# Optimization experiments

Hardware: AMD Instinct MI355X
Metric: run time of the kernel (lower is better)

Reference implementation:

```python
import jax, jax.numpy as jnp
import numpy as np

N, C_A, C_S, C_Z, H = 1024, 768, 384, 128, 16
D = C_A // H  # 48


def _ln(x, gamma=None, beta=None, eps=1e-5):
    m = jnp.mean(x, axis=-1, keepdims=True)
    v = jnp.var(x, axis=-1, keepdims=True)
    y = (x - m) * jax.lax.rsqrt(v + eps)
    if gamma is not None:
        y = y * gamma
    if beta is not None:
        y = y + beta
    return y


def _adaln(a, s, gamma_s, Wg, bg, Wadd):
    # AF3 Algorithm 26: LN(a) w/o affine, LN(s) w/ scale only; gate + additive shift from s
    a_ln = _ln(a)
    s_ln = _ln(s, gamma_s)
    return jax.nn.sigmoid(s_ln @ Wg + bg) * a_ln + s_ln @ Wadd


def setup_inputs() -> dict:
    key = jax.random.key(0)
    ks = iter(jax.random.split(key, 40))
    def nrm(shape, scale=0.02):
        return jax.random.normal(next(ks), shape, dtype=jnp.float32) * scale
    f32 = jnp.float32
    return dict(
        a=jax.random.normal(next(ks), (1, N, C_A), dtype=f32),
        s=jax.random.normal(next(ks), (1, N, C_S), dtype=f32),
        z=jax.random.normal(next(ks), (1, N, N, C_Z), dtype=f32),
        # AdaptiveLayerNorm (attention branch)
        gamma_s1=jnp.ones((C_S,), f32), Wg1=nrm((C_S, C_A)), bg1=jnp.zeros((C_A,), f32), Wadd1=nrm((C_S, C_A)),
        # pair-bias: LN(z) scale-only + LinearNoBias(c_z -> n_heads)
        gamma_z=jnp.ones((C_Z,), f32), Wz=nrm((C_Z, H)),
        # Attention: q has bias, k/v no bias, sigmoid gating, output proj
        Wq=nrm((C_A, C_A)), bq=jnp.zeros((C_A,), f32),
        Wk=nrm((C_A, C_A)), Wv=nrm((C_A, C_A)),
        Wgate=nrm((C_A, C_A)), bgate=jnp.ones((C_A,), f32),
        Wo=nrm((C_A, C_A)), bo=jnp.zeros((C_A,), f32),
        # BiasInitLinear output gate (biasinit=-2)
        Ws_last=nrm((C_S, C_A)), bs_last=jnp.full((C_A,), -2.0, f32),
        # ConditionedTransitionBlock (n=2)
        gamma_s2=jnp.ones((C_S,), f32), Wg2=nrm((C_S, C_A)), bg2=jnp.zeros((C_A,), f32), Wadd2=nrm((C_S, C_A)),
        W1=nrm((C_A, 2 * C_A)), W2=nrm((C_A, 2 * C_A)), Wb=nrm((2 * C_A, C_A)),
        Ws_t=nrm((C_S, C_A)), b_t=jnp.full((C_A,), -2.0, f32),
    )


def reference(a, s, z, gamma_s1, Wg1, bg1, Wadd1, gamma_z, Wz,
              Wq, bq, Wk, Wv, Wgate, bgate, Wo, bo, Ws_last, bs_last,
              gamma_s2, Wg2, bg2, Wadd2, W1, W2, Wb, Ws_t, b_t):
    B = a.shape[0]
    # ---- AttentionPairBias (standard / global path) ----
    a_ln = _adaln(a, s, gamma_s1, Wg1, bg1, Wadd1)
    bias = _ln(z, gamma_z) @ Wz                     # [B, N, N, H]
    bias = jnp.moveaxis(bias, -1, -3)               # [B, H, N, N]
    q = (a_ln @ Wq + bq).reshape(B, N, H, D)
    k = (a_ln @ Wk).reshape(B, N, H, D)
    v = (a_ln @ Wv).reshape(B, N, H, D)
    scale = 1.0 / float(np.sqrt(D))
    scores = jnp.einsum('bqhd,bkhd->bhqk', q, k) * scale + bias
    attn = jax.nn.softmax(scores, axis=-1)
    o = jnp.einsum('bhqk,bkhd->bqhd', attn, v)      # [B, N, H, D]
    g = jax.nn.sigmoid(a_ln @ Wgate + bgate).reshape(B, N, H, D)
    o = (g * o).reshape(B, N, C_A) @ Wo + bo
    attn_out = jax.nn.sigmoid(s @ Ws_last + bs_last) * o
    # ---- ConditionedTransitionBlock (Algorithm 25, n=2) ----
    a2 = _adaln(a, s, gamma_s2, Wg2, bg2, Wadd2)
    bmid = jax.nn.silu(a2 @ W1) * (a2 @ W2)
    t_out = jax.nn.sigmoid(s @ Ws_t + b_t) * (bmid @ Wb)
    # Algorithm 23 line 2-3: a = b + ConditionedTransitionBlock(a, s)
    return attn_out + t_out
```

## Files before the change

kernel.cpp:

```cpp
#include <hip/hip_runtime.h>

typedef __bf16 bf16;
typedef __bf16 v8bf __attribute__((ext_vector_type(8)));
typedef float  v4f  __attribute__((ext_vector_type(4)));
typedef short  short4v __attribute__((ext_vector_type(4)));

__device__ __forceinline__ float sigf(float x){ return 1.0f/(1.0f + __expf(-x)); }

typedef __attribute__((address_space(3))) unsigned int lds_u32;
typedef __attribute__((address_space(1))) const unsigned int gbl_u32;
__device__ __forceinline__ void gl16(const void* g, void* l) {
  __builtin_amdgcn_global_load_lds((gbl_u32*)g, (lds_u32*)l, 16, 0, 0);
}

struct WTab {
  const float* src[14];
  bf16* dst[14];
  int K[14], N[14], boff[14];
};

__device__ __forceinline__ void prepw_body(int bid, char* smem, const WTab& tab) {
  float (*lds)[33] = (float(*)[33])smem;
  int e = 0;
  #pragma unroll
  for (int i = 1; i < 14; i++) if (tab.boff[i] <= bid) e = i;
  int local = bid - tab.boff[e];
  int K = tab.K[e], N = tab.N[e];
  int nKT = K >> 5;
  int kt = local % nKT, nt = local / nKT;
  int k0 = kt * 32, n0 = nt * 32;
  const float* src = tab.src[e];
  bf16* dst = tab.dst[e];
  int tx = threadIdx.x & 31, ty = threadIdx.x >> 5;
  #pragma unroll
  for (int i = 0; i < 4; i++)
    lds[ty + i*8][tx] = src[(long)(k0 + ty + i*8) * N + n0 + tx];
  __syncthreads();
  #pragma unroll
  for (int i = 0; i < 4; i++)
    dst[(long)(n0 + ty + i*8) * K + k0 + tx] = (bf16)lds[tx][ty + i*8];
}

__device__ __forceinline__ void ln_a_body(int row, const float* __restrict__ a,
                                          float* __restrict__ out) {
  const float* x = a + (long)row * 768;
  int t = threadIdx.x;
  float lv[3], s = 0.f, q = 0.f;
  #pragma unroll
  for (int i = 0; i < 3; i++){ lv[i] = x[t + i*256]; s += lv[i]; q += lv[i]*lv[i]; }
  #pragma unroll
  for (int m = 1; m < 64; m <<= 1){ s += __shfl_xor(s, m); q += __shfl_xor(q, m); }
  __shared__ float ls[4], lq[4];
  int w = t >> 6, lane = t & 63;
  if (!lane){ ls[w] = s; lq[w] = q; }
  __syncthreads();
  s = ls[0]+ls[1]+ls[2]+ls[3]; q = lq[0]+lq[1]+lq[2]+lq[3];
  float mean = s * (1.f/768.f);
  float var  = q * (1.f/768.f) - mean*mean;
  float inv  = rsqrtf(var + 1e-5f);
  float* o = out + (long)row * 768;
  #pragma unroll
  for (int i = 0; i < 3; i++) o[t + i*256] = (lv[i] - mean) * inv;
}

__device__ __forceinline__ void ln_s_body(int rowpair, const float* __restrict__ sIn,
    const float* __restrict__ g1, const float* __restrict__ g2,
    bf16* __restrict__ s1, bf16* __restrict__ s2, bf16* __restrict__ sb) {
  int t = threadIdx.x & 127;
  int sub = threadIdx.x >> 7;
  int r = rowpair*2 + sub;
  const float* x = sIn + (long)r * 384;
  float lv[3], s = 0.f, q = 0.f;
  #pragma unroll
  for (int i = 0; i < 3; i++){ lv[i] = x[t + i*128]; s += lv[i]; q += lv[i]*lv[i]; }
  #pragma unroll
  for (int m = 1; m < 64; m <<= 1){ s += __shfl_xor(s, m); q += __shfl_xor(q, m); }
  __shared__ float ls[2][2], lq[2][2];
  int w = (t >> 6) & 1, lane = t & 63;
  if (!lane){ ls[sub][w] = s; lq[sub][w] = q; }
  __syncthreads();
  s = ls[sub][0] + ls[sub][1]; q = lq[sub][0] + lq[sub][1];
  float mean = s * (1.f/384.f);
  float var  = q * (1.f/384.f) - mean*mean;
  float inv  = rsqrtf(var + 1e-5f);
  long base = (long)r * 384;
  #pragma unroll
  for (int i = 0; i < 3; i++){
    int c = t + i*128;
    float y = (lv[i] - mean) * inv;
    s1[base + c] = (bf16)(y * g1[c]);
    s2[base + c] = (bf16)(y * g2[c]);
    sb[base + c] = (bf16)lv[i];
  }
}

__global__ __launch_bounds__(256) void k_prep(WTab tab, int boffTot,
    const float* Wz, const float* gz, bf16* wzT,
    const float* A_in, float* alnr,
    const float* S_in, const float* g1, const float* g2,
    bf16* sl1, bf16* sl2, bf16* sbf)
{
  __shared__ __align__(16) char smem[4224];
  int bid = blockIdx.x;
  if (bid < boffTot) { prepw_body(bid, smem, tab); return; }
  bid -= boffTot;
  if (bid < 8) {
    int t = bid * 256 + threadIdx.x;
    int k = t >> 4, h = t & 15;
    wzT[h * 128 + k] = (bf16)(Wz[t] * gz[k]);
    return;
  }
  bid -= 8;
  if (bid < 1024) { ln_a_body(bid, A_in, alnr); return; }
  bid -= 1024;
  ln_s_body(bid, S_in, g1, g2, sl1, sl2, sbf);
}

__device__ __forceinline__ void zbias_body(int bid, char* smem,
    const float* __restrict__ z, const bf16* __restrict__ wzT,
    bf16* __restrict__ biasb) {
  float (*pb)[17] = (float(*)[17])smem;
  int t = threadIdx.x, lane = t & 63, w = t >> 6;
  int r16 = lane & 15, g4 = lane >> 4;
  long base = (long)bid * 64;
  long pos = base + w*16 + r16;
  const float* zr = z + pos * 128;
  float4 xv[8];
  #pragma unroll
  for (int s = 0; s < 4; s++) {
    xv[2*s]   = *reinterpret_cast<const float4*>(&zr[s*32 + g4*8]);
    xv[2*s+1] = *reinterpret_cast<const float4*>(&zr[s*32 + g4*8 + 4]);
  }
  const float* x = reinterpret_cast<const float*>(xv);
  float sm = 0.f, q = 0.f;
  #pragma unroll
  for (int i = 0; i < 32; i++){ sm += x[i]; q += x[i]*x[i]; }
  sm += __shfl_xor(sm, 16); q += __shfl_xor(q, 16);
  sm += __shfl_xor(sm, 32); q += __shfl_xor(q, 32);
  float mean = sm * (1.f/128.f), var = q * (1.f/128.f) - mean*mean;
  float inv = rsqrtf(var + 1e-5f);
  v4f acc = (v4f){0.f, 0.f, 0.f, 0.f};
  #pragma unroll
  for (int s = 0; s < 4; s++) {
    union { bf16 b[8]; v8bf v; } ua;
    #pragma unroll
    for (int j = 0; j < 8; j++) ua.b[j] = (bf16)((x[s*8 + j] - mean) * inv);
    v8bf bw = *reinterpret_cast<const v8bf*>(&wzT[r16*128 + s*32 + g4*8]);
    acc = __builtin_amdgcn_mfma_f32_16x16x32_bf16(ua.v, bw, acc, 0, 0, 0);
  }
  #pragma unroll
  for (int r = 0; r < 4; r++) pb[w*16 + g4*4 + r][r16] = acc[r];
  __syncthreads();
  int p = t & 63, hb = t >> 6;
  #pragma unroll
  for (int j = 0; j < 4; j++) {
    int h = hb*4 + j;
    biasb[((long)h << 20) + base + p] = (bf16)pb[p][h];
  }
}

#define EPI_ADASG  0
#define EPI_SWIGLU 1
#define EPI_QKVG   2
#define EPI_WO     6
#define EPI_WB     7

template<int TM, int TN, bool DUAL, int EPI>
__device__ __forceinline__ void gemm_body(
    bf16* As, bf16* Bs, int m0, int n0, int z,
    const bf16* __restrict__ Ap, const bf16* __restrict__ B1, long sBpair, int K,
    const float* __restrict__ f0, const float* __restrict__ f1,
    const float* __restrict__ f2, const float* __restrict__ f3,
    const float* __restrict__ f4, const bf16* __restrict__ bb0,
    void* __restrict__ outp, long sOutz)
{
  constexpr int WM = TM/2, WN = TN/2;
  constexpr int MI = WM/16, NI = WN/16;
  const bf16* B2 = B1 + sBpair;
  int t = threadIdx.x, lane = t & 63, w = t >> 6;
  int wr = w >> 1, wc = w & 1;
  int r16 = lane & 15, g4 = lane >> 4;
  constexpr int NACC = DUAL ? 2 : 1;
  v4f acc[NACC][MI][NI];
  #pragma unroll
  for (int d = 0; d < NACC; d++)
    #pragma unroll
    for (int mi = 0; mi < MI; mi++)
      #pragma unroll
      for (int ni = 0; ni < NI; ni++)
        acc[d][mi][ni] = (v4f){0.f, 0.f, 0.f, 0.f};

  for (int k0 = 0; k0 < K; k0 += 64) {
    #pragma unroll
    for (int cb = 0; cb < TM/32; cb++) {
      int cc = cb*4 + w;
      int c16 = cc*64 + lane;
      int row = c16 >> 3, col = c16 & 7;
      int scol = col ^ (row & 7);
      gl16(&Ap[(long)(m0 + row)*K + k0 + scol*8], (char*)As + cc*1024);
    }
    #pragma unroll
    for (int cb = 0; cb < TN/32; cb++) {
      int cc = cb*4 + w;
      int c16 = cc*64 + lane;
      int row = c16 >> 3, col = c16 & 7;
      int scol = col ^ (row & 7);
      gl16(&B1[(long)(n0 + row)*K + k0 + scol*8], (char*)Bs + cc*1024);
      if constexpr (DUAL)
        gl16(&B2[(long)(n0 + row)*K + k0 + scol*8], (char*)Bs + TN*128 + cc*1024);
    }
    __syncthreads();
    #pragma unroll
    for (int s = 0; s < 2; s++) {
      int ch = s*4 + g4;
      v8bf af[MI];
      #pragma unroll
      for (int mi = 0; mi < MI; mi++) {
        int ra = wr*WM + mi*16 + r16;
        af[mi] = *reinterpret_cast<const v8bf*>(
            (const char*)As + ra*128 + ((ch ^ (ra & 7)) << 4));
      }
      #pragma unroll
      for (int d = 0; d < NACC; d++)
        #pragma unroll
        for (int ni = 0; ni < NI; ni++) {
          int rb = wc*WN + ni*16 + r16;
          v8bf bfv = *reinterpret_cast<const v8bf*>(
              (const char*)Bs + d*(TN*128) + rb*128 + ((ch ^ (rb & 7)) << 4));
          #pragma unroll
          for (int mi = 0; mi < MI; mi++)
            acc[d][mi][ni] = __builtin_amdgcn_mfma_f32_16x16x32_bf16(af[mi], bfv, acc[d][mi][ni], 0, 0, 0);
        }
    }
    __syncthreads();
  }

  int colb = n0 + wc*WN + r16;
  int rowb = m0 + wr*WM + (g4 << 2);
  #pragma unroll
  for (int mi = 0; mi < MI; mi++)
    #pragma unroll
    for (int ni = 0; ni < NI; ni++) {
      int col = colb + ni*16;
      if constexpr (EPI == EPI_ADASG) {
        if (z < 2) {
          float bg = (z == 0 ? f1 : f2)[col];
          bf16* o = (bf16*)outp + (long)z * sOutz;
          #pragma unroll
          for (int r = 0; r < 4; r++) {
            long idx = (long)(rowb + mi*16 + r)*768 + col;
            float gl = acc[0][mi][ni][r] + bg;
            o[idx] = (bf16)(sigf(gl) * f0[idx] + acc[1][mi][ni][r]);
          }
        } else {
          bf16* o0 = (bf16*)outp + 2*sOutz;
          bf16* o1 = (bf16*)outp + 3*sOutz;
          #pragma unroll
          for (int r = 0; r < 4; r++) {
            long idx = (long)(rowb + mi*16 + r)*768 + col;
            o0[idx] = (bf16)sigf(acc[0][mi][ni][r] + f3[col]);
            o1[idx] = (bf16)sigf(acc[1][mi][ni][r] + f4[col]);
          }
        }
      } else if constexpr (EPI == EPI_SWIGLU) {
        bf16* o = (bf16*)outp;
        #pragma unroll
        for (int r = 0; r < 4; r++) {
          long idx = (long)(rowb + mi*16 + r)*1536 + col;
          float x1 = acc[0][mi][ni][r], x2 = acc[1][mi][ni][r];
          o[idx] = (bf16)(x1 * sigf(x1) * x2);
        }
      } else if constexpr (EPI == EPI_QKVG) {
        int h = col / 48, d = col - h*48;
        if (z == 0) {
          const float qs = 0.14433756729740643f;
          bf16* qp = (bf16*)outp;
          #pragma unroll
          for (int r = 0; r < 4; r++)
            qp[(long)h*65536 + (long)(rowb + mi*16 + r)*64 + d] =
              (bf16)((acc[0][mi][ni][r] + f0[col]) * qs);
        } else if (z == 1) {
          bf16* kp = (bf16*)outp + sOutz;
          #pragma unroll
          for (int r = 0; r < 4; r++)
            kp[(long)h*65536 + (long)(rowb + mi*16 + r)*64 + d] = (bf16)acc[0][mi][ni][r];
        } else if (z == 2) {
          bf16* vT = (bf16*)outp + 2*sOutz;
          union { bf16 h4[4]; short4v s4; } u;
          #pragma unroll
          for (int r = 0; r < 4; r++) u.h4[r] = (bf16)acc[0][mi][ni][r];
          *reinterpret_cast<short4v*>(&vT[(long)h*65536 + (long)d*1024 + rowb + mi*16]) = u.s4;
        } else {
          bf16* gp = (bf16*)outp + 3*sOutz;
          #pragma unroll
          for (int r = 0; r < 4; r++)
            gp[(long)(rowb + mi*16 + r)*768 + col] = (bf16)sigf(acc[0][mi][ni][r] + f1[col]);
        }
      } else if constexpr (EPI == EPI_WO) {
        float* o = (float*)outp;
        #pragma unroll
        for (int r = 0; r < 4; r++) {
          long idx = (long)(rowb + mi*16 + r)*768 + col;
          o[idx] = (float)bb0[idx] * (acc[0][mi][ni][r] + f0[col]);
        }
      } else {
        float* o = (float*)outp;
        #pragma unroll
        for (int r = 0; r < 4; r++) {
          long idx = (long)(rowb + mi*16 + r)*768 + col;
          o[idx] = f0[idx] + (float)bb0[idx] * acc[0][mi][ni][r];
        }
      }
    }
}

template<int TM, int TN, bool DUAL, int EPI>
__global__ __launch_bounds__(256) void gemm_k(
    const bf16* A, const bf16* B, long sAz, long sBz, long sBpair, int K,
    const float* f0, const float* f1, const float* f2, const float* f3,
    const float* f4, const bf16* bb0, void* outp, long sOutz)
{
  __shared__ __align__(16) bf16 As[TM*64];
  __shared__ __align__(16) bf16 Bs[(DUAL?2:1)*TN*64];
  int z = blockIdx.z;
  gemm_body<TM,TN,DUAL,EPI>(As, Bs, blockIdx.y*TM, blockIdx.x*TN, z,
      A + (long)z*sAz, B + (long)z*sBz, sBpair, K,
      f0, f1, f2, f3, f4, bb0, outp, sOutz);
}

#define ZSPLIT 5120

__global__ __launch_bounds__(256, 4) void k_mega_a(
    const bf16* sl1, const bf16* wGA6, const float* alnr,
    const float* bg1, const float* bg2, const float* bsL, const float* b_t,
    bf16* aln, const float* Zin, const bf16* wzT, bf16* biasb)
{
  __shared__ __align__(16) char smem[24576];
  int bid = blockIdx.x;
  if (bid < 576) {
    int z = bid / 192, rem = bid % 192;
    gemm_body<64,64,true,EPI_ADASG>((bf16*)smem, (bf16*)(smem + 8192),
        (rem/12)*64, (rem%12)*64, z,
        sl1 + (long)z*393216, wGA6 + (long)z*589824, 294912, 384,
        alnr, bg1, bg2, bsL, b_t, nullptr, aln, 786432);
  } else {
    zbias_body(bid - 576, smem, Zin, wzT, biasb);
  }
}

__global__ __launch_bounds__(256, 3) void k_mega_b(
    const bf16* aln, const bf16* wQKVG, const float* bq, const float* bgate,
    bf16* qkv, const bf16* a2b, const bf16* wW12, bf16* bmid,
    const float* Zin, const bf16* wzT, bf16* biasb)
{
  __shared__ __align__(16) char smem[32768];
  int bid = blockIdx.x;
  if (bid < 192) {
    int z = bid / 48, rem = bid % 48;
    gemm_body<128,128,false,EPI_QKVG>((bf16*)smem, (bf16*)(smem + 16384),
        (rem/6)*128, (rem%6)*128, z,
        aln, wQKVG + (long)z*589824, 0, 768,
        bq, bgate, nullptr, nullptr, nullptr, nullptr, qkv, 1048576);
  } else if (bid < 576) {
    int rem = bid - 192;
    gemm_body<64,64,true,EPI_SWIGLU>((bf16*)smem, (bf16*)(smem + 8192),
        (rem/24)*64, (rem%24)*64, 0,
        a2b, wW12, 1179648, 768,
        nullptr, nullptr, nullptr, nullptr, nullptr, nullptr, bmid, 0);
  } else {
    zbias_body(bid - 576 + ZSPLIT, smem, Zin, wzT, biasb);
  }
}

__global__ __launch_bounds__(256) void k_flash(
    const bf16* __restrict__ qp, const bf16* __restrict__ kp,
    const bf16* __restrict__ vT, const bf16* __restrict__ biasb,
    const bf16* __restrict__ gp, bf16* __restrict__ gob)
{
  __shared__ bf16 pl[4][16*72];
  int t = threadIdx.x, lane = t & 63, w = t >> 6;
  int h = blockIdx.y;
  int q0 = blockIdx.x * 64 + w * 16;
  int r16 = lane & 15, g4 = lane >> 4;
  const bf16* qb = qp + ((long)h << 16);
  const bf16* kb = kp + ((long)h << 16);
  const bf16* vb = vT + ((long)h << 16);
  const bf16* bb = biasb + ((long)h << 20) + (long)q0 * 1024;

  v8bf qa[2];
  #pragma unroll
  for (int s = 0; s < 2; s++)
    qa[s] = *reinterpret_cast<const v8bf*>(&qb[(long)(q0 + r16)*64 + s*32 + g4*8]);

  v4f oacc[4];
  #pragma unroll
  for (int nd = 0; nd < 4; nd++) oacc[nd] = (v4f){0.f, 0.f, 0.f, 0.f};
  float mrun[4], lrun[4];
  #pragma unroll
  for (int r = 0; r < 4; r++){ mrun[r] = -1e30f; lrun[r] = 0.f; }

  for (int kt = 0; kt < 16; kt++) {
    int k0 = kt * 64;
    v4f sacc[4];
    #pragma unroll
    for (int nk = 0; nk < 4; nk++) sacc[nk] = (v4f){0.f, 0.f, 0.f, 0.f};
    #pragma unroll
    for (int nk = 0; nk < 4; nk++)
      #pragma unroll
      for (int s = 0; s < 2; s++) {
        v8bf kf = *reinterpret_cast<const v8bf*>(&kb[(long)(k0 + nk*16 + r16)*64 + s*32 + g4*8]);
        sacc[nk] = __builtin_amdgcn_mfma_f32_16x16x32_bf16(qa[s], kf, sacc[nk], 0, 0, 0);
      }
    float mtile[4];
    #pragma unroll
    for (int r = 0; r < 4; r++) mtile[r] = -1e30f;
    #pragma unroll
    for (int nk = 0; nk < 4; nk++)
      #pragma unroll
      for (int r = 0; r < 4; r++) {
        float bvv = (float)bb[(long)(g4*4 + r)*1024 + k0 + nk*16 + r16];
        sacc[nk][r] += bvv;
        mtile[r] = fmaxf(mtile[r], sacc[nk][r]);
      }
    #pragma unroll
    for (int r = 0; r < 4; r++) {
      #pragma unroll
      for (int m = 1; m < 16; m <<= 1) mtile[r] = fmaxf(mtile[r], __shfl_xor(mtile[r], m));
    }
    float scl[4], rsum[4];
    #pragma unroll
    for (int r = 0; r < 4; r++) {
      float mn = fmaxf(mrun[r], mtile[r]);
      scl[r] = __expf(mrun[r] - mn);
      mrun[r] = mn;
      rsum[r] = 0.f;
    }
    bf16* plw = &pl[w][0];
    #pragma unroll
    for (int nk = 0; nk < 4; nk++)
      #pragma unroll
      for (int r = 0; r < 4; r++) {
        float p = __expf(sacc[nk][r] - mrun[r]);
        rsum[r] += p;
        plw[(g4*4 + r)*72 + nk*16 + r16] = (bf16)p;
      }
    #pragma unroll
    for (int r = 0; r < 4; r++) {
      #pragma unroll
      for (int m = 1; m < 16; m <<= 1) rsum[r] += __shfl_xor(rsum[r], m);
      lrun[r] = lrun[r]*scl[r] + rsum[r];
      #pragma unroll
      for (int nd = 0; nd < 4; nd++) oacc[nd][r] *= scl[r];
    }
    v8bf pa[2];
    #pragma unroll
    for (int s = 0; s < 2; s++)
      pa[s] = *reinterpret_cast<const v8bf*>(&plw[r16*72 + s*32 + g4*8]);
    #pragma unroll
    for (int nd = 0; nd < 4; nd++)
      #pragma unroll
      for (int s = 0; s < 2; s++) {
        v8bf vf = *reinterpret_cast<const v8bf*>(&vb[(long)(nd*16 + r16)*1024 + k0 + s*32 + g4*8]);
        oacc[nd] = __builtin_amdgcn_mfma_f32_16x16x32_bf16(pa[s], vf, oacc[nd], 0, 0, 0);
      }
  }
  #pragma unroll
  for (int r = 0; r < 4; r++) {
    int qrow = q0 + g4*4 + r;
    float invl = 1.0f / lrun[r];
    #pragma unroll
    for (int nd = 0; nd < 3; nd++) {
      long idx = (long)qrow*768 + h*48 + nd*16 + r16;
      gob[idx] = (bf16)(oacc[nd][r] * invl * (float)gp[idx]);
    }
  }
}

extern "C" void kernel_launch(void* const* d_in, const int* in_sizes, int n_in,
                              void* d_out, int out_size, void* d_ws, size_t ws_size,
                              hipStream_t stream)
{
  const float* A_in  = (const float*)d_in[0];
  const float* S_in  = (const float*)d_in[1];
  const float* Z_in  = (const float*)d_in[2];
  const float* g_s1  = (const float*)d_in[3];
  const float* Wg1   = (const float*)d_in[4];
  const float* bg1   = (const float*)d_in[5];
  const float* Wadd1 = (const float*)d_in[6];
  const float* g_z   = (const float*)d_in[7];
  const float* Wz    = (const float*)d_in[8];
  const float* Wq    = (const float*)d_in[9];
  const float* bq    = (const float*)d_in[10];
  const float* Wk    = (const float*)d_in[11];
  const float* Wv    = (const float*)d_in[12];
  const float* Wgate = (const float*)d_in[13];
  const float* bgate = (const float*)d_in[14];
  const float* Wo    = (const float*)d_in[15];
  const float* bo    = (const float*)d_in[16];
  const float* WsL   = (const float*)d_in[17];
  const float* bsL   = (const float*)d_in[18];
  const float* g_s2  = (const float*)d_in[19];
  const float* Wg2   = (const float*)d_in[20];
  const float* bg2   = (const float*)d_in[21];
  const float* Wadd2 = (const float*)d_in[22];
  const float* W1    = (const float*)d_in[23];
  const float* W2    = (const float*)d_in[24];
  const float* Wb    = (const float*)d_in[25];
  const float* WsT   = (const float*)d_in[26];
  const float* b_t   = (const float*)d_in[27];
  float* OUT = (float*)d_out;

  char* ws = (char*)d_ws;
  size_t off = 0;
  auto alloc = [&](size_t bytes) -> void* {
    void* p = ws + off; off += (bytes + 255) & ~(size_t)255; return p; };

  bf16*  wGA6  = (bf16*) alloc(6ul*294912*2);
  bf16*  wQKVG = (bf16*) alloc(4ul*589824*2);
  bf16*  wWoT  = (bf16*) alloc(589824ul*2);
  bf16*  wW12  = (bf16*) alloc(2ul*1179648*2);
  bf16*  wWbT  = (bf16*) alloc(1179648ul*2);
  bf16*  wzT   = (bf16*) alloc(2048ul*2);
  bf16*  sl1   = (bf16*) alloc(393216ul*2);
  bf16*  sl2   = (bf16*) alloc(393216ul*2);
  bf16*  sbf   = (bf16*) alloc(393216ul*2);
  float* alnr  = (float*)alloc(786432ul*4);
  bf16*  aln   = (bf16*) alloc(786432ul*2);
  bf16*  a2b   = (bf16*) alloc(786432ul*2);
  bf16*  sgf   = (bf16*) alloc(2ul*786432*2);
  bf16*  qkv   = (bf16*) alloc((3ul*1048576 + 786432)*2);
  bf16*  biasb = (bf16*) alloc(16777216ul*2);
  bf16*  gob   = (bf16*) alloc(786432ul*2);
  float* opj   = (float*)alloc(786432ul*4);
  bf16*  bmid  = (bf16*) alloc(1572864ul*2);

  WTab tab;
  auto setw = [&](int i, const float* src, bf16* dst, int K, int N){
    tab.src[i] = src; tab.dst[i] = dst; tab.K[i] = K; tab.N[i] = N; };
  setw(0,  Wg1,   wGA6,             384,  768);
  setw(1,  Wadd1, wGA6 + 294912,    384,  768);
  setw(2,  Wg2,   wGA6 + 589824,    384,  768);
  setw(3,  Wadd2, wGA6 + 884736,    384,  768);
  setw(4,  WsL,   wGA6 + 1179648,   384,  768);
  setw(5,  WsT,   wGA6 + 1474560,   384,  768);
  setw(6,  Wq,    wQKVG,            768,  768);
  setw(7,  Wk,    wQKVG + 589824,   768,  768);
  setw(8,  Wv,    wQKVG + 2*589824, 768,  768);
  setw(9,  Wgate, wQKVG + 3*589824, 768,  768);
  setw(10, Wo,    wWoT,             768,  768);
  setw(11, W1,    wW12,             768, 1536);
  setw(12, W2,    wW12 + 1179648,   768, 1536);
  setw(13, Wb,    wWbT,            1536,  768);
  int boff = 0;
  for (int i = 0; i < 14; i++){ tab.boff[i] = boff; boff += (tab.K[i]/32)*(tab.N[i]/32); }

  (void)hipMemsetAsync(qkv, 0, 3ul*1048576*2, stream);

  k_prep<<<boff + 8 + 1024 + 512, 256, 0, stream>>>(
      tab, boff, Wz, g_z, wzT, A_in, alnr, S_in, g_s1, g_s2, sl1, sl2, sbf);

  k_mega_a<<<576 + ZSPLIT, 256, 0, stream>>>(
      sl1, wGA6, alnr, bg1, bg2, bsL, b_t, aln, Z_in, wzT, biasb);

  k_mega_b<<<576 + (16384 - ZSPLIT), 256, 0, stream>>>(
      aln, wQKVG, bq, bgate, qkv, a2b, wW12, bmid, Z_in, wzT, biasb);

  k_flash<<<dim3(16,16), 256, 0, stream>>>(
      qkv, qkv + 1048576, qkv + 2097152, biasb, qkv + 3145728, gob);

  gemm_k<64,64,false,EPI_WO><<<dim3(12,16,1), 256, 0, stream>>>(
      gob, wWoT, 0, 0, 0, 768,
      bo, nullptr, nullptr, nullptr, nullptr, sgf, opj, 0);

  gemm_k<64,64,false,EPI_WB><<<dim3(12,16,1), 256, 0, stream>>>(
      bmid, wWbT, 0, 0, 0, 1536,
      opj, nullptr, nullptr, nullptr, nullptr, sgf + 786432, OUT, 0);
}
```

Baseline: 232.8 us.

## Co-schedule Wb GEMM with flash attention in one tail launch, accumulate Wo into output

Merges the independent transition-block Wb GEMM and the flash attention into a single launch of 448 blocks (192 GEMM tiles plus 256 attention tiles), so the two share the GPU at the same time and one kernel launch goes away. The Wb GEMM now writes its gated result directly to the output. The Wo GEMM then runs afterwards and adds its gated result to the output in place, which removes the opj intermediate buffer and its write and read. The cost is a read-modify-write on the output and an ordering dependency between the two writes to it. The flash tiles also move to a shared-memory allocation sized for the GEMM (16 KB), which may affect occupancy.

After: 262.1 us. +12.6%, slower.

```diff
diff --git a/kernel.cpp b/kernel.cpp
--- a/kernel.cpp
+++ b/kernel.cpp
@@ -301,14 +301,14 @@
         #pragma unroll
         for (int r = 0; r < 4; r++) {
           long idx = (long)(rowb + mi*16 + r)*768 + col;
-          o[idx] = (float)bb0[idx] * (acc[0][mi][ni][r] + f0[col]);
+          o[idx] = o[idx] + (float)bb0[idx] * (acc[0][mi][ni][r] + f0[col]);
         }
       } else {
         float* o = (float*)outp;
         #pragma unroll
         for (int r = 0; r < 4; r++) {
           long idx = (long)(rowb + mi*16 + r)*768 + col;
-          o[idx] = f0[idx] + (float)bb0[idx] * acc[0][mi][ni][r];
+          o[idx] = (float)bb0[idx] * acc[0][mi][ni][r];
         }
       }
     }
@@ -372,16 +372,15 @@
   }
 }
 
-__global__ __launch_bounds__(256) void k_flash(
+__device__ __forceinline__ void flash_body(int qt, int h, char* smem,
     const bf16* __restrict__ qp, const bf16* __restrict__ kp,
     const bf16* __restrict__ vT, const bf16* __restrict__ biasb,
     const bf16* __restrict__ gp, bf16* __restrict__ gob)
 {
-  __shared__ bf16 pl[4][16*72];
   int t = threadIdx.x, lane = t & 63, w = t >> 6;
-  int h = blockIdx.y;
-  int q0 = blockIdx.x * 64 + w * 16;
+  int q0 = qt * 64 + w * 16;
   int r16 = lane & 15, g4 = lane >> 4;
+  bf16* plw = (bf16*)smem + w * 1152;
   const bf16* qb = qp + ((long)h << 16);
   const bf16* kb = kp + ((long)h << 16);
   const bf16* vb = vT + ((long)h << 16);
@@ -435,7 +434,6 @@
       mrun[r] = mn;
       rsum[r] = 0.f;
     }
-    bf16* plw = &pl[w][0];
     #pragma unroll
     for (int nk = 0; nk < 4; nk++)
       #pragma unroll
@@ -473,6 +471,24 @@
       long idx = (long)qrow*768 + h*48 + nd*16 + r16;
       gob[idx] = (bf16)(oacc[nd][r] * invl * (float)gp[idx]);
     }
+  }
+}
+
+__global__ __launch_bounds__(256) void k_tail(
+    const bf16* bmid, const bf16* wWbT, const bf16* sgf1, float* OUT,
+    const bf16* qp, const bf16* kp, const bf16* vT, const bf16* biasb,
+    const bf16* gp, bf16* gob)
+{
+  __shared__ __align__(16) char smem[16384];
+  int bid = blockIdx.x;
+  if (bid < 192) {
+    gemm_body<64,64,false,EPI_WB>((bf16*)smem, (bf16*)(smem + 8192),
+        (bid/12)*64, (bid%12)*64, 0,
+        bmid, wWbT, 0, 1536,
+        nullptr, nullptr, nullptr, nullptr, nullptr, sgf1, OUT, 0);
+  } else {
+    int local = bid - 192;
+    flash_body(local & 15, local >> 4, smem, qp, kp, vT, biasb, gp, gob);
   }
 }
 
@@ -531,7 +547,6 @@
   bf16*  qkv   = (bf16*) alloc((3ul*1048576 + 786432)*2);
   bf16*  biasb = (bf16*) alloc(16777216ul*2);
   bf16*  gob   = (bf16*) alloc(786432ul*2);
-  float* opj   = (float*)alloc(786432ul*4);
   bf16*  bmid  = (bf16*) alloc(1572864ul*2);
 
   WTab tab;
@@ -565,14 +580,11 @@
   k_mega_b<<<576 + (16384 - ZSPLIT), 256, 0, stream>>>(
       aln, wQKVG, bq, bgate, qkv, a2b, wW12, bmid, Z_in, wzT, biasb);
 
-  k_flash<<<dim3(16,16), 256, 0, stream>>>(
+  k_tail<<<448, 256, 0, stream>>>(
+      bmid, wWbT, sgf + 786432, OUT,
       qkv, qkv + 1048576, qkv + 2097152, biasb, qkv + 3145728, gob);
 
   gemm_k<64,64,false,EPI_WO><<<dim3(12,16,1), 256, 0, stream>>>(
       gob, wWoT, 0, 0, 0, 768,
-      bo, nullptr, nullptr, nullptr, nullptr, sgf, opj, 0);
-
-  gemm_k<64,64,false,EPI_WB><<<dim3(12,16,1), 256, 0, stream>>>(
-      bmid, wWbT, 0, 0, 0, 1536,
-      opj, nullptr, nullptr, nullptr, nullptr, sgf + 786432, OUT, 0);
-}
+      bo, nullptr, nullptr, nullptr, nullptr, sgf, OUT, 0);
+}
```
